# Kernel tuning notes

Measured on AMD Instinct MI355X. Metric: run time of the kernel, lower is better.

Reference implementation:

```python
import jax, jax.numpy as jnp
import numpy as np

N_NODES = 100000
N_EDGES = 1600000
IN_DIM, HID_DIM, OUT_DIM = 256, 128, 128


def gcn_norm(edge_index, edge_weight, num_nodes):
    # Add self-loops with weight 1 (PyG GCNConv default fill_value=1.0)
    loop = jnp.arange(num_nodes, dtype=edge_index.dtype)
    src = jnp.concatenate([edge_index[0], loop])
    dst = jnp.concatenate([edge_index[1], loop])
    w = jnp.concatenate([edge_weight, jnp.ones((num_nodes,), edge_weight.dtype)])
    # Symmetric normalization: deg computed at destination over edge weights
    deg = jax.ops.segment_sum(w, dst, num_segments=num_nodes)
    dinv = jnp.where(deg > 0, jax.lax.rsqrt(deg), 0.0)
    norm = dinv[src] * w * dinv[dst]  # [E + N]
    return src, dst, norm


def gcn_conv(x, W, b, src, dst, norm, num_nodes):
    h = x @ W                                  # [N, out]
    msg = h[src] * norm[:, None]               # gather + scale, [E+N, out]
    out = jax.ops.segment_sum(msg, dst, num_segments=num_nodes)  # scatter-add
    return out + b


def setup_inputs() -> dict:
    key = jax.random.key(0)
    ks = jax.random.split(key, 8)
    x = jax.random.normal(ks[0], (N_NODES, IN_DIM), dtype=jnp.float32)
    edge_index = jax.random.randint(ks[1], (2, N_EDGES), 0, N_NODES, dtype=jnp.int64)
    edge_weight = jax.random.uniform(ks[2], (N_EDGES,), dtype=jnp.float32)
    s1 = 1.0 / np.sqrt(IN_DIM)
    s2 = 1.0 / np.sqrt(HID_DIM)
    W1 = jax.random.uniform(ks[3], (IN_DIM, HID_DIM), jnp.float32, -s1, s1)
    b1 = jnp.zeros((HID_DIM,), jnp.float32)
    W2 = jax.random.uniform(ks[4], (HID_DIM, OUT_DIM), jnp.float32, -s2, s2)
    b2 = jnp.zeros((OUT_DIM,), jnp.float32)
    return {"x": x, "edge_index": edge_index, "edge_weight": edge_weight,
            "W1": W1, "b1": b1, "W2": W2, "b2": b2}


def reference(x, edge_index, edge_weight, W1, b1, W2, b2):
    n = x.shape[0]
    src, dst, norm = gcn_norm(edge_index, edge_weight, n)
    h = jax.nn.relu(gcn_conv(x, W1, b1, src, dst, norm, n))
    out = gcn_conv(h, W2, b2, src, dst, norm, n)
    return out
```

## Files before the change

kernel.cpp:

```cpp
#include <hip/hip_runtime.h>
#include <stdint.h>

#define N_NODES 100000
#define N_EDGES 1600000
#define IN_DIM 256
#define HID_DIM 128
#define OUT_DIM 128

#define NBUCK 391
#define CHUNK 4096

typedef __attribute__((ext_vector_type(8))) short short8;
typedef __attribute__((ext_vector_type(4))) float floatx4;

__device__ __forceinline__ float bf2f(unsigned short u) {
    union { unsigned int i; float f; } v; v.i = ((unsigned int)u) << 16; return v.f;
}
__device__ __forceinline__ unsigned short f2bf(float f) {
    union { float fl; unsigned int i; } v; v.fl = f;
    unsigned int x = v.i;
    return (unsigned short)((x + 0x7fffu + ((x >> 16) & 1u)) >> 16);
}
__device__ __forceinline__ float bflo(unsigned int u) {
    union { unsigned int i; float f; } v; v.i = u << 16; return v.f;
}
__device__ __forceinline__ float bfhi(unsigned int u) {
    union { unsigned int i; float f; } v; v.i = u & 0xffff0000u; return v.f;
}
__device__ __forceinline__ float asf(unsigned int u) {
    union { unsigned int i; float f; } v; v.i = u; return v.f;
}
__device__ __forceinline__ unsigned int asu(float f) {
    union { float fl; unsigned int i; } v; v.fl = f; return v.i;
}
__device__ __forceinline__ unsigned int pack2(float a, float b) {
    unsigned int ua = asu(a), ub = asu(b);
    ua += 0x7fffu + ((ua >> 16) & 1u);
    ub += 0x7fffu + ((ub >> 16) & 1u);
    return (ua >> 16) | (ub & 0xffff0000u);
}
__device__ __forceinline__ short8 pack8(float4 a, float4 b) {
    union { unsigned int u[4]; short8 s; } r;
    r.u[0] = pack2(a.x, a.y);
    r.u[1] = pack2(a.z, a.w);
    r.u[2] = pack2(b.x, b.y);
    r.u[3] = pack2(b.z, b.w);
    return r.s;
}

__global__ void k_detect(const unsigned int* __restrict__ xu, const unsigned int* __restrict__ eu,
                         int* __restrict__ flags, int* __restrict__ bucket_cnt) {
    __shared__ int s_huge, s_odd;
    if (threadIdx.x == 0) { s_huge = 0; s_odd = 0; }
    if (threadIdx.x < NBUCK) bucket_cnt[threadIdx.x] = 0;
    __syncthreads();
    int huge = 0, odd = 0;
    for (int i = threadIdx.x; i < 1024; i += 512) {
        unsigned int b = xu[i];
        unsigned int e = (b >> 23) & 0xffu;
        if (e >= 0xf0u) huge = 1;
        if (eu[2 * i + 1] != 0) odd = 1;
    }
    if (huge) atomicOr(&s_huge, 1);
    if (odd) atomicOr(&s_odd, 1);
    __syncthreads();
    if (threadIdx.x == 0) { flags[0] = s_huge ? 0 : 1; flags[1] = s_odd ? 0 : 1; }
}

__device__ __forceinline__ int load_idx(const void* base, long long i, int i64m) {
    int v = i64m ? (int)((const long long*)base)[i] : ((const int*)base)[i];
    return v < 0 ? 0 : (v >= N_NODES ? N_NODES - 1 : v);
}
__device__ __forceinline__ float load_f(const void* base, long long i, int f32m) {
    return f32m ? ((const float*)base)[i] : bf2f(((const unsigned short*)base)[i]);
}

__global__ void k_bhist(const void* __restrict__ ei, const int* __restrict__ flags,
                        int* __restrict__ bucket_cnt, int e) {
    __shared__ int h[NBUCK];
    for (int t = threadIdx.x; t < NBUCK; t += 256) h[t] = 0;
    __syncthreads();
    int i64m = flags[1];
    int base = blockIdx.x * CHUNK;
    int end = base + CHUNK < e ? base + CHUNK : e;
    for (int i = base + threadIdx.x; i < end; i += 256) {
        int d = load_idx(ei, (long long)N_EDGES + i, i64m);
        atomicAdd(&h[d >> 8], 1);
    }
    __syncthreads();
    for (int t = threadIdx.x; t < NBUCK; t += 256)
        if (h[t]) atomicAdd(&bucket_cnt[t], h[t]);
}

__global__ void k_bscan(const int* __restrict__ bucket_cnt, int* __restrict__ bucket_base,
                        int* __restrict__ bucket_cursor, int* __restrict__ rowptr) {
    __shared__ int lds[512];
    int t = threadIdx.x;
    int v = (t < NBUCK) ? bucket_cnt[t] : 0;
    lds[t] = v;
    __syncthreads();
    for (int off = 1; off < 512; off <<= 1) {
        int x = (t >= off) ? lds[t - off] : 0;
        __syncthreads();
        lds[t] += x;
        __syncthreads();
    }
    int excl = lds[t] - v;
    if (t < NBUCK) { bucket_base[t] = excl; bucket_cursor[t] = excl; }
    if (t == 0) { bucket_base[NBUCK] = lds[NBUCK - 1]; rowptr[N_NODES] = N_EDGES; }
}

__global__ void k_bscatter(const void* __restrict__ ei, const void* __restrict__ ew,
                           const int* __restrict__ flags, int* __restrict__ bucket_cursor,
                           uint2* __restrict__ ebuf, int e) {
    __shared__ int h[NBUCK];
    for (int t = threadIdx.x; t < NBUCK; t += 256) h[t] = 0;
    __syncthreads();
    int f32m = flags[0], i64m = flags[1];
    int base = blockIdx.x * CHUNK;
    int end = base + CHUNK < e ? base + CHUNK : e;
    for (int i = base + threadIdx.x; i < end; i += 256) {
        int d = load_idx(ei, (long long)N_EDGES + i, i64m);
        atomicAdd(&h[d >> 8], 1);
    }
    __syncthreads();
    for (int t = threadIdx.x; t < NBUCK; t += 256) {
        int c = h[t];
        h[t] = c ? atomicAdd(&bucket_cursor[t], c) : 0;
    }
    __syncthreads();
    for (int i = base + threadIdx.x; i < end; i += 256) {
        int s = load_idx(ei, i, i64m);
        int d = load_idx(ei, (long long)N_EDGES + i, i64m);
        float w = load_f(ew, i, f32m);
        int b = d >> 8;
        int p = atomicAdd(&h[b], 1);
        uint2 c; c.x = (unsigned int)s | ((unsigned int)(d & 255) << 17); c.y = asu(w);
        ebuf[p] = c;
    }
}

__global__ void k_fine(const uint2* __restrict__ ebuf, const int* __restrict__ bucket_base,
                       uint2* __restrict__ csr, int* __restrict__ rowptr,
                       float* __restrict__ dinv, int n) {
    __shared__ int h[256];
    __shared__ float fw[256];
    __shared__ int c2[256];
    int t = threadIdx.x, b = blockIdx.x;
    int e0 = bucket_base[b], e1 = bucket_base[b + 1];
    h[t] = 0; fw[t] = 0.f;
    __syncthreads();
    for (int i = e0 + t; i < e1; i += 256) {
        uint2 c = ebuf[i];
        int dl = (c.x >> 17) & 255;
        atomicAdd(&h[dl], 1);
        atomicAdd(&fw[dl], asf(c.y));
    }
    __syncthreads();
    int own = h[t];
    for (int off = 1; off < 256; off <<= 1) {
        int x = (t >= off) ? h[t - off] : 0;
        __syncthreads();
        h[t] += x;
        __syncthreads();
    }
    int excl = h[t] - own;
    int node = (b << 8) + t;
    if (node < n) {
        rowptr[node] = e0 + excl;
        dinv[node] = rsqrtf(1.0f + fw[t]);
    }
    c2[t] = e0 + excl;
    __syncthreads();
    for (int i = e0 + t; i < e1; i += 256) {
        uint2 c = ebuf[i];
        int dl = (c.x >> 17) & 255;
        int p = atomicAdd(&c2[dl], 1);
        csr[p] = c;
    }
}

__global__ void k_fold(uint4* __restrict__ csr4, const float* __restrict__ dinv, int npair) {
    int i = blockIdx.x * 256 + threadIdx.x;
    if (i >= npair) return;
    uint4 c = csr4[i];
    c.y = asu(asf(c.y) * dinv[c.x & 0x1FFFF]);
    c.w = asu(asf(c.w) * dinv[c.z & 0x1FFFF]);
    csr4[i] = c;
}

__global__ void k_transpose(const void* __restrict__ W1, const void* __restrict__ W2,
                            const int* __restrict__ flags,
                            unsigned short* __restrict__ W1T, unsigned short* __restrict__ W2T) {
    int i = blockIdx.x * 256 + threadIdx.x;
    int f32m = flags[0];
    if (i < IN_DIM * HID_DIM) {
        int k = i / HID_DIM, n = i % HID_DIM;
        W1T[n * IN_DIM + k] = f2bf(load_f(W1, i, f32m));
    } else {
        int j = i - IN_DIM * HID_DIM;
        if (j < HID_DIM * OUT_DIM) {
            int k = j / OUT_DIM, n = j % OUT_DIM;
            W2T[n * HID_DIM + k] = f2bf(load_f(W2, j, f32m));
        }
    }
}

template <int KH, bool F32M>
__device__ __forceinline__ void gemm_loop(const void* __restrict__ A,
                                          const unsigned short* __restrict__ Bs,
                                          size_t aoff0, size_t aoff1,
                                          int quad, int l16, floatx4 (&acc)[2][8]) {
    constexpr int NCH = KH / 32;
    constexpr int BMASK = KH / 8 - 1;
    float4 fraw[2][2];
    short8 braw[2];
    if (F32M) {
        const float* ap = (const float*)A;
        fraw[0][0] = *(const float4*)(ap + aoff0);
        fraw[0][1] = *(const float4*)(ap + aoff0 + 4);
        fraw[1][0] = *(const float4*)(ap + aoff1);
        fraw[1][1] = *(const float4*)(ap + aoff1 + 4);
    } else {
        const unsigned short* ap = (const unsigned short*)A;
        braw[0] = *(const short8*)(ap + aoff0);
        braw[1] = *(const short8*)(ap + aoff1);
    }
#pragma unroll
    for (int ch = 0; ch < NCH; ch++) {
        float4 nf[2][2];
        short8 nb[2];
        if (ch + 1 < NCH) {
            int o = (ch + 1) * 32;
            if (F32M) {
                const float* ap = (const float*)A;
                nf[0][0] = *(const float4*)(ap + aoff0 + o);
                nf[0][1] = *(const float4*)(ap + aoff0 + o + 4);
                nf[1][0] = *(const float4*)(ap + aoff1 + o);
                nf[1][1] = *(const float4*)(ap + aoff1 + o + 4);
            } else {
                const unsigned short* ap = (const unsigned short*)A;
                nb[0] = *(const short8*)(ap + aoff0 + o);
                nb[1] = *(const short8*)(ap + aoff1 + o);
            }
        }
        short8 a0, a1;
        if (F32M) {
            a0 = pack8(fraw[0][0], fraw[0][1]);
            a1 = pack8(fraw[1][0], fraw[1][1]);
        } else {
            a0 = braw[0];
            a1 = braw[1];
        }
#pragma unroll
        for (int c = 0; c < 8; c++) {
            int col = c * 16 + l16;
            int boff = col * KH + 8 * ((ch * 4 + quad + (col & 7)) & BMASK);
            short8 bf = *(const short8*)(Bs + boff);
            acc[0][c] = __builtin_amdgcn_mfma_f32_16x16x32_bf16(a0, bf, acc[0][c], 0, 0, 0);
            acc[1][c] = __builtin_amdgcn_mfma_f32_16x16x32_bf16(a1, bf, acc[1][c], 0, 0, 0);
        }
        if (ch + 1 < NCH) {
            if (F32M) {
                fraw[0][0] = nf[0][0]; fraw[0][1] = nf[0][1];
                fraw[1][0] = nf[1][0]; fraw[1][1] = nf[1][1];
            } else {
                braw[0] = nb[0]; braw[1] = nb[1];
            }
        }
    }
}

template <int K, bool RAWA>
__global__ void k_gemm(const void* __restrict__ A, const unsigned short* __restrict__ WT,
                       unsigned short* __restrict__ H, const int* __restrict__ flags, int n) {
    constexpr int KH = (K > 128) ? 128 : K;
    __shared__ unsigned short Bs[128 * KH];

    int wave = threadIdx.x >> 6;
    int lane = threadIdx.x & 63;
    int quad = lane >> 4;
    int l16 = lane & 15;
    int rowbase = blockIdx.x * 128 + wave * 32;
    int r0 = rowbase + l16;        if (r0 >= n) r0 = n - 1;
    int r1 = rowbase + 16 + l16;   if (r1 >= n) r1 = n - 1;
    size_t aoff0 = (size_t)r0 * K + quad * 8;
    size_t aoff1 = (size_t)r1 * K + quad * 8;

    floatx4 acc[2][8];
#pragma unroll
    for (int t = 0; t < 2; t++)
#pragma unroll
        for (int c = 0; c < 8; c++) acc[t][c] = (floatx4){0.f, 0.f, 0.f, 0.f};

    int f32m = RAWA ? flags[0] : 0;

#pragma unroll
    for (int hh = 0; hh < K / KH; hh++) {
        if (hh) __syncthreads();
        for (int base = threadIdx.x * 8; base < 128 * KH; base += 256 * 8) {
            int col = base / KH;
            int k = base - col * KH;
            int ks = (k + (col & 7) * 8) & (KH - 1);
            *(short8*)(&Bs[col * KH + ks]) = *(const short8*)(WT + col * K + hh * KH + k);
        }
        __syncthreads();
        if (RAWA && f32m)
            gemm_loop<KH, true>(A, Bs, aoff0 + hh * KH, aoff1 + hh * KH, quad, l16, acc);
        else
            gemm_loop<KH, false>(A, Bs, aoff0 + hh * KH, aoff1 + hh * KH, quad, l16, acc);
    }

#pragma unroll
    for (int t = 0; t < 2; t++)
#pragma unroll
        for (int c = 0; c < 8; c++)
#pragma unroll
            for (int r = 0; r < 4; r++) {
                int grow = rowbase + t * 16 + quad * 4 + r;
                if (grow < n) H[(size_t)grow * 128 + c * 16 + l16] = f2bf(acc[t][c][r]);
            }
}

#define NODES_PER_BLK 64

__device__ __forceinline__ void acc8(float wt, uint4 hv, float* a) {
    a[0] += wt * bflo(hv.x); a[1] += wt * bfhi(hv.x);
    a[2] += wt * bflo(hv.y); a[3] += wt * bfhi(hv.y);
    a[4] += wt * bflo(hv.z); a[5] += wt * bfhi(hv.z);
    a[6] += wt * bflo(hv.w); a[7] += wt * bfhi(hv.w);
}

template <bool RELU, bool FINAL>
__global__ void k_aggregate(const unsigned short* __restrict__ H, const int* __restrict__ rowptr,
                            const uint2* __restrict__ csr, const float* __restrict__ dinv,
                            const void* __restrict__ bias, void* __restrict__ out,
                            const int* __restrict__ flags, int n) {
    __shared__ int cursor;
    if (threadIdx.x == 0) cursor = 0;
    __syncthreads();
    int lane = threadIdx.x & 15;
    int col = lane * 8;
    int f32m = flags[0];

    float bv[8];
#pragma unroll
    for (int i = 0; i < 8; i++) bv[i] = load_f(bias, col + i, f32m);

    for (;;) {
        int idx;
        if (lane == 0) idx = atomicAdd(&cursor, 1);
        idx = __shfl(idx, 0, 16);
        if (idx >= NODES_PER_BLK) break;
        int node = blockIdx.x * NODES_PER_BLK + idx;
        if (node >= n) break;

        int e0 = rowptr[node], e1 = rowptr[node + 1];
        uint4 u = *(const uint4*)(H + (size_t)node * 128 + col);
        float dn = dinv[node];

        float a[8] = {0.f, 0.f, 0.f, 0.f, 0.f, 0.f, 0.f, 0.f};
        int e = e0;
        for (; e + 4 <= e1; e += 4) {
            uint2 c0 = csr[e], c1 = csr[e + 1], c2 = csr[e + 2], c3 = csr[e + 3];
            uint4 h0 = *(const uint4*)(H + (size_t)(c0.x & 0x1FFFF) * 128 + col);
            uint4 h1 = *(const uint4*)(H + (size_t)(c1.x & 0x1FFFF) * 128 + col);
            uint4 h2 = *(const uint4*)(H + (size_t)(c2.x & 0x1FFFF) * 128 + col);
            uint4 h3 = *(const uint4*)(H + (size_t)(c3.x & 0x1FFFF) * 128 + col);
            acc8(asf(c0.y), h0, a); acc8(asf(c1.y), h1, a);
            acc8(asf(c2.y), h2, a); acc8(asf(c3.y), h3, a);
        }
        for (; e < e1; e++) {
            uint2 c = csr[e];
            uint4 hh = *(const uint4*)(H + (size_t)(c.x & 0x1FFFF) * 128 + col);
            acc8(asf(c.y), hh, a);
        }

        float coef = dn * dn;
        a[0] = dn * a[0] + coef * bflo(u.x) + bv[0];
        a[1] = dn * a[1] + coef * bfhi(u.x) + bv[1];
        a[2] = dn * a[2] + coef * bflo(u.y) + bv[2];
        a[3] = dn * a[3] + coef * bfhi(u.y) + bv[3];
        a[4] = dn * a[4] + coef * bflo(u.z) + bv[4];
        a[5] = dn * a[5] + coef * bfhi(u.z) + bv[5];
        a[6] = dn * a[6] + coef * bflo(u.w) + bv[6];
        a[7] = dn * a[7] + coef * bfhi(u.w) + bv[7];

        if (RELU) {
#pragma unroll
            for (int i = 0; i < 8; i++) a[i] = fmaxf(a[i], 0.f);
        }
        if (FINAL && f32m) {
            float* op = (float*)out + (size_t)node * 128 + col;
            float4 o0 = {a[0], a[1], a[2], a[3]};
            float4 o1 = {a[4], a[5], a[6], a[7]};
            *(float4*)op = o0;
            *(float4*)(op + 4) = o1;
        } else {
            uint4 o;
            o.x = pack2(a[0], a[1]); o.y = pack2(a[2], a[3]);
            o.z = pack2(a[4], a[5]); o.w = pack2(a[6], a[7]);
            *(uint4*)((unsigned short*)out + (size_t)node * 128 + col) = o;
        }
    }
}

extern "C" void kernel_launch(void* const* d_in, const int* in_sizes, int n_in,
                              void* d_out, int out_size, void* d_ws, size_t ws_size,
                              hipStream_t stream) {
    const void* x  = d_in[0];
    const void* ei = d_in[1];
    const void* ew = d_in[2];
    const void* W1 = d_in[3];
    const void* b1 = d_in[4];
    const void* W2 = d_in[5];
    const void* b2 = d_in[6];

    char* p = (char*)d_ws;
    auto alloc = [&](size_t bytes) { char* r = p; p += (bytes + 255) & ~(size_t)255; return r; };
    int*   flags    = (int*)alloc(256);
    float* dinv     = (float*)alloc((size_t)N_NODES * 4);
    int*   rowptr   = (int*)alloc((size_t)(N_NODES + 1) * 4);
    int*   bucket_cnt    = (int*)alloc((size_t)NBUCK * 4);
    int*   bucket_base   = (int*)alloc((size_t)(NBUCK + 1) * 4);
    int*   bucket_cursor = (int*)alloc((size_t)NBUCK * 4);
    uint2* csr      = (uint2*)alloc((size_t)N_EDGES * 8);
    unsigned short* W1T  = (unsigned short*)alloc((size_t)IN_DIM * HID_DIM * 2);
    unsigned short* W2T  = (unsigned short*)alloc((size_t)HID_DIM * OUT_DIM * 2);
    unsigned short* hbuf = (unsigned short*)alloc((size_t)N_NODES * 128 * 2);
    unsigned short* zbuf = (unsigned short*)alloc((size_t)N_NODES * 128 * 2);
    uint2* ebuf = (uint2*)hbuf;

    int nbC = (N_EDGES + CHUNK - 1) / CHUNK;
    int nbG = (N_NODES + 127) / 128;
    int nbA = (N_NODES + NODES_PER_BLK - 1) / NODES_PER_BLK;
    int nbF = (N_EDGES / 2 + 255) / 256;

    k_detect<<<1, 512, 0, stream>>>((const unsigned int*)x, (const unsigned int*)ei, flags, bucket_cnt);
    k_bhist<<<nbC, 256, 0, stream>>>(ei, flags, bucket_cnt, N_EDGES);
    k_bscan<<<1, 512, 0, stream>>>(bucket_cnt, bucket_base, bucket_cursor, rowptr);
    k_bscatter<<<nbC, 256, 0, stream>>>(ei, ew, flags, bucket_cursor, ebuf, N_EDGES);
    k_fine<<<NBUCK, 256, 0, stream>>>(ebuf, bucket_base, csr, rowptr, dinv, N_NODES);
    k_fold<<<nbF, 256, 0, stream>>>((uint4*)csr, dinv, N_EDGES / 2);
    k_transpose<<<(IN_DIM * HID_DIM + HID_DIM * OUT_DIM + 255) / 256, 256, 0, stream>>>(W1, W2, flags, W1T, W2T);

    k_gemm<IN_DIM, true><<<nbG, 256, 0, stream>>>(x, W1T, hbuf, flags, N_NODES);
    k_aggregate<true, false><<<nbA, 256, 0, stream>>>(hbuf, rowptr, csr, dinv,
                                                      b1, zbuf, flags, N_NODES);
    k_gemm<HID_DIM, false><<<nbG, 256, 0, stream>>>(zbuf, W2T, hbuf, flags, N_NODES);
    k_aggregate<false, true><<<nbA, 256, 0, stream>>>(hbuf, rowptr, csr, dinv,
                                                      b2, d_out, flags, N_NODES);
}
```

Before: 454.4 us.

## Shrink GEMM and aggregate tiles, widen fine-sort blocks, halve chunk size

The GEMM now computes one 16-row tile per wave instead of two, so each block covers 64 rows and twice as many blocks launch. All A chunks are preloaded up front instead of being double-buffered. The fine bucket sort runs with 512 threads per block, with the scan guarded to the first 256 threads. The bucket histogram and scatter chunks are halved, and the aggregation handles fewer nodes per block, to raise parallelism and occupancy. In exchange, each GEMM block reuses its shared-memory weight tile across fewer rows, and more blocks and launches add overhead.

New measurement: 447.7 us. Within noise of the previous version (-1.5%).

```diff
diff --git a/kernel.cpp b/kernel.cpp
--- a/kernel.cpp
+++ b/kernel.cpp
@@ -8,7 +8,7 @@
 #define OUT_DIM 128
 
 #define NBUCK 391
-#define CHUNK 4096
+#define CHUNK 2048
 
 typedef __attribute__((ext_vector_type(8))) short short8;
 typedef __attribute__((ext_vector_type(4))) float floatx4;
@@ -148,31 +148,33 @@
     __shared__ int c2[256];
     int t = threadIdx.x, b = blockIdx.x;
     int e0 = bucket_base[b], e1 = bucket_base[b + 1];
-    h[t] = 0; fw[t] = 0.f;
-    __syncthreads();
-    for (int i = e0 + t; i < e1; i += 256) {
+    if (t < 256) { h[t] = 0; fw[t] = 0.f; }
+    __syncthreads();
+    for (int i = e0 + t; i < e1; i += 512) {
         uint2 c = ebuf[i];
         int dl = (c.x >> 17) & 255;
         atomicAdd(&h[dl], 1);
         atomicAdd(&fw[dl], asf(c.y));
     }
     __syncthreads();
-    int own = h[t];
+    int own = (t < 256) ? h[t] : 0;
     for (int off = 1; off < 256; off <<= 1) {
-        int x = (t >= off) ? h[t - off] : 0;
+        int x = (t >= off && t < 256) ? h[t - off] : 0;
         __syncthreads();
-        h[t] += x;
+        if (t < 256) h[t] += x;
         __syncthreads();
     }
-    int excl = h[t] - own;
-    int node = (b << 8) + t;
-    if (node < n) {
-        rowptr[node] = e0 + excl;
-        dinv[node] = rsqrtf(1.0f + fw[t]);
-    }
-    c2[t] = e0 + excl;
-    __syncthreads();
-    for (int i = e0 + t; i < e1; i += 256) {
+    if (t < 256) {
+        int excl = h[t] - own;
+        int node = (b << 8) + t;
+        if (node < n) {
+            rowptr[node] = e0 + excl;
+            dinv[node] = rsqrtf(1.0f + fw[t]);
+        }
+        c2[t] = e0 + excl;
+    }
+    __syncthreads();
+    for (int i = e0 + t; i < e1; i += 512) {
         uint2 c = ebuf[i];
         int dl = (c.x >> 17) & 255;
         int p = atomicAdd(&c2[dl], 1);
@@ -209,64 +211,32 @@
 template <int KH, bool F32M>
 __device__ __forceinline__ void gemm_loop(const void* __restrict__ A,
                                           const unsigned short* __restrict__ Bs,
-                                          size_t aoff0, size_t aoff1,
-                                          int quad, int l16, floatx4 (&acc)[2][8]) {
+                                          size_t aoff, int quad, int l16, floatx4 (&acc)[8]) {
     constexpr int NCH = KH / 32;
     constexpr int BMASK = KH / 8 - 1;
-    float4 fraw[2][2];
-    short8 braw[2];
+    short8 a[NCH];
     if (F32M) {
         const float* ap = (const float*)A;
-        fraw[0][0] = *(const float4*)(ap + aoff0);
-        fraw[0][1] = *(const float4*)(ap + aoff0 + 4);
-        fraw[1][0] = *(const float4*)(ap + aoff1);
-        fraw[1][1] = *(const float4*)(ap + aoff1 + 4);
+#pragma unroll
+        for (int ch = 0; ch < NCH; ch++) {
+            float4 f0 = *(const float4*)(ap + aoff + ch * 32);
+            float4 f1 = *(const float4*)(ap + aoff + ch * 32 + 4);
+            a[ch] = pack8(f0, f1);
+        }
     } else {
         const unsigned short* ap = (const unsigned short*)A;
-        braw[0] = *(const short8*)(ap + aoff0);
-        braw[1] = *(const short8*)(ap + aoff1);
+#pragma unroll
+        for (int ch = 0; ch < NCH; ch++)
+            a[ch] = *(const short8*)(ap + aoff + ch * 32);
     }
 #pragma unroll
     for (int ch = 0; ch < NCH; ch++) {
-        float4 nf[2][2];
-        short8 nb[2];
-        if (ch + 1 < NCH) {
-            int o = (ch + 1) * 32;
-            if (F32M) {
-                const float* ap = (const float*)A;
-                nf[0][0] = *(const float4*)(ap + aoff0 + o);
-                nf[0][1] = *(const float4*)(ap + aoff0 + o + 4);
-                nf[1][0] = *(const float4*)(ap + aoff1 + o);
-                nf[1][1] = *(const float4*)(ap + aoff1 + o + 4);
-            } else {
-                const unsigned short* ap = (const unsigned short*)A;
-                nb[0] = *(const short8*)(ap + aoff0 + o);
-                nb[1] = *(const short8*)(ap + aoff1 + o);
-            }
-        }
-        short8 a0, a1;
-        if (F32M) {
-            a0 = pack8(fraw[0][0], fraw[0][1]);
-            a1 = pack8(fraw[1][0], fraw[1][1]);
-        } else {
-            a0 = braw[0];
-            a1 = braw[1];
-        }
 #pragma unroll
         for (int c = 0; c < 8; c++) {
             int col = c * 16 + l16;
             int boff = col * KH + 8 * ((ch * 4 + quad + (col & 7)) & BMASK);
             short8 bf = *(const short8*)(Bs + boff);
-            acc[0][c] = __builtin_amdgcn_mfma_f32_16x16x32_bf16(a0, bf, acc[0][c], 0, 0, 0);
-            acc[1][c] = __builtin_amdgcn_mfma_f32_16x16x32_bf16(a1, bf, acc[1][c], 0, 0, 0);
-        }
-        if (ch + 1 < NCH) {
-            if (F32M) {
-                fraw[0][0] = nf[0][0]; fraw[0][1] = nf[0][1];
-                fraw[1][0] = nf[1][0]; fraw[1][1] = nf[1][1];
-            } else {
-                braw[0] = nb[0]; braw[1] = nb[1];
-            }
+            acc[c] = __builtin_amdgcn_mfma_f32_16x16x32_bf16(a[ch], bf, acc[c], 0, 0, 0);
         }
     }
 }
@@ -281,17 +251,13 @@
     int lane = threadIdx.x & 63;
     int quad = lane >> 4;
     int l16 = lane & 15;
-    int rowbase = blockIdx.x * 128 + wave * 32;
+    int rowbase = blockIdx.x * 64 + wave * 16;
     int r0 = rowbase + l16;        if (r0 >= n) r0 = n - 1;
-    int r1 = rowbase + 16 + l16;   if (r1 >= n) r1 = n - 1;
     size_t aoff0 = (size_t)r0 * K + quad * 8;
-    size_t aoff1 = (size_t)r1 * K + quad * 8;
-
-    floatx4 acc[2][8];
-#pragma unroll
-    for (int t = 0; t < 2; t++)
-#pragma unroll
-        for (int c = 0; c < 8; c++) acc[t][c] = (floatx4){0.f, 0.f, 0.f, 0.f};
+
+    floatx4 acc[8];
+#pragma unroll
+    for (int c = 0; c < 8; c++) acc[c] = (floatx4){0.f, 0.f, 0.f, 0.f};
 
     int f32m = RAWA ? flags[0] : 0;
 
@@ -306,23 +272,21 @@
         }
         __syncthreads();
         if (RAWA && f32m)
-            gemm_loop<KH, true>(A, Bs, aoff0 + hh * KH, aoff1 + hh * KH, quad, l16, acc);
+            gemm_loop<KH, true>(A, Bs, aoff0 + hh * KH, quad, l16, acc);
         else
-            gemm_loop<KH, false>(A, Bs, aoff0 + hh * KH, aoff1 + hh * KH, quad, l16, acc);
-    }
-
-#pragma unroll
-    for (int t = 0; t < 2; t++)
-#pragma unroll
-        for (int c = 0; c < 8; c++)
-#pragma unroll
-            for (int r = 0; r < 4; r++) {
-                int grow = rowbase + t * 16 + quad * 4 + r;
-                if (grow < n) H[(size_t)grow * 128 + c * 16 + l16] = f2bf(acc[t][c][r]);
-            }
-}
-
-#define NODES_PER_BLK 64
+            gemm_loop<KH, false>(A, Bs, aoff0 + hh * KH, quad, l16, acc);
+    }
+
+#pragma unroll
+    for (int c = 0; c < 8; c++)
+#pragma unroll
+        for (int r = 0; r < 4; r++) {
+            int grow = rowbase + quad * 4 + r;
+            if (grow < n) H[(size_t)grow * 128 + c * 16 + l16] = f2bf(acc[c][r]);
+        }
+}
+
+#define NODES_PER_BLK 32
 
 __device__ __forceinline__ void acc8(float wt, uint4 hv, float* a) {
     a[0] += wt * bflo(hv.x); a[1] += wt * bfhi(hv.x);
@@ -432,7 +396,7 @@
     uint2* ebuf = (uint2*)hbuf;
 
     int nbC = (N_EDGES + CHUNK - 1) / CHUNK;
-    int nbG = (N_NODES + 127) / 128;
+    int nbG = (N_NODES + 63) / 64;
     int nbA = (N_NODES + NODES_PER_BLK - 1) / NODES_PER_BLK;
     int nbF = (N_EDGES / 2 + 255) / 256;
 
@@ -440,7 +404,7 @@
     k_bhist<<<nbC, 256, 0, stream>>>(ei, flags, bucket_cnt, N_EDGES);
     k_bscan<<<1, 512, 0, stream>>>(bucket_cnt, bucket_base, bucket_cursor, rowptr);
     k_bscatter<<<nbC, 256, 0, stream>>>(ei, ew, flags, bucket_cursor, ebuf, N_EDGES);
-    k_fine<<<NBUCK, 256, 0, stream>>>(ebuf, bucket_base, csr, rowptr, dinv, N_NODES);
+    k_fine<<<NBUCK, 512, 0, stream>>>(ebuf, bucket_base, csr, rowptr, dinv, N_NODES);
     k_fold<<<nbF, 256, 0, stream>>>((uint4*)csr, dinv, N_EDGES / 2);
     k_transpose<<<(IN_DIM * HID_DIM + HID_DIM * OUT_DIM + 255) / 256, 256, 0, stream>>>(W1, W2, flags, W1T, W2T);
 
```
